# Kernel tuning notes

Measured on AMD Instinct MI355X. Metric: run time of the kernel, lower is better.

The kernel has to match this reference:

```python
import jax, jax.numpy as jnp
import numpy as np
import math

B, N, C = 1, 2048, 256
H, CH = 8, 32
PQ, PV = 8, 12
CZ = 32
BQ, BK = 32, 128
NB = N // BQ
PAD = (BK - BQ) // 2
INF = 1e8
EPS = 1e-8

_KIDX = np.arange(NB)[:, None] * BQ + np.arange(BK)[None, :] - PAD
_KVALID = (_KIDX >= 0) & (_KIDX < N)
_KIDX_C = np.clip(_KIDX, 0, N - 1)


def _quat_to_rot(q):
    q = q / jnp.linalg.norm(q, axis=-1, keepdims=True)
    w, x, y, z = q[..., 0], q[..., 1], q[..., 2], q[..., 3]
    return jnp.stack([
        jnp.stack([1 - 2 * (y * y + z * z), 2 * (x * y - w * z), 2 * (x * z + w * y)], -1),
        jnp.stack([2 * (x * y + w * z), 1 - 2 * (x * x + z * z), 2 * (y * z - w * x)], -1),
        jnp.stack([2 * (x * z - w * y), 2 * (y * z + w * x), 1 - 2 * (x * x + y * y)], -1)], -2)


def _to_queries(x):
    # [B, N, ...] -> [B, NB, BQ, ...]
    return x.reshape((B, NB, BQ) + x.shape[2:])


def _to_keys(x):
    # [B, N, ...] -> [B, NB, BK, ...] zero-padded sliding key windows
    g = x[:, _KIDX_C]
    v = jnp.asarray(_KVALID, x.dtype).reshape((1, NB, BK) + (1,) * (x.ndim - 2))
    return g * v


def _ln(x):
    m = x.mean(-1, keepdims=True)
    var = x.var(-1, keepdims=True)
    return (x - m) / jnp.sqrt(var + 1e-5)


def setup_inputs():
    key = jax.random.key(0)
    ks = jax.random.split(key, 16)
    p = 0.02
    return {
        's': jax.random.normal(ks[0], (B, N, C), jnp.float32),
        'cond': jax.random.normal(ks[1], (B, N, C), jnp.float32),
        'z': jax.random.normal(ks[2], (B, NB, BQ, BK, CZ), jnp.float32),
        'trans': jax.random.normal(ks[3], (B, N, 3), jnp.float32),
        'rots': _quat_to_rot(jax.random.normal(ks[4], (B, N, 4), jnp.float32)),
        's_mask': jnp.ones((B, N), jnp.float32),
        'Wq': jax.random.normal(ks[5], (C, H * CH)) * p,
        'Wk': jax.random.normal(ks[6], (C, H * CH)) * p,
        'Wv': jax.random.normal(ks[7], (C, H * CH)) * p,
        'Wqp': jax.random.normal(ks[8], (C, H * PQ * 3)) * p,
        'Wkvp': jax.random.normal(ks[9], (C, H * (PQ + PV) * 3)) * p,
        'Wb': jax.random.normal(ks[10], (CZ, H)) * p,
        'Wdz': jax.random.normal(ks[11], (CZ, CZ // 4)) * p,
        'head_weights': jnp.full((H,), 0.5413),
        'Wout': jax.random.normal(ks[12], (H * (CZ // 4 + CH + PV * 4), C)) * p,
        'Wg': jax.random.normal(ks[13], (C, C)) * p,
        'bg': jnp.zeros((C,)),
        'Wbeta': jax.random.normal(ks[14], (C, C)) * p,
        'bbeta': jnp.zeros((C,)),
        'g_z': jnp.ones((CZ,)),
        'b_z': jnp.zeros((CZ,)),
    }


def reference(s, cond, z, trans, rots, s_mask, Wq, Wk, Wv, Wqp, Wkvp, Wb, Wdz,
              head_weights, Wout, Wg, bg, Wbeta, bbeta, g_z, b_z):
    # AdaLN on s conditioned on cond; LayerNorm on z
    s = _ln(s) * (cond @ Wg + bg) + (cond @ Wbeta + bbeta)
    z = _ln(z) * g_z + b_z

    q_in = _to_queries(s)            # [B,NB,BQ,C]
    k_in = _to_keys(s)               # [B,NB,BK,C]
    q_t = _to_queries(trans)         # [B,NB,BQ,3]
    q_R = _to_queries(rots)          # [B,NB,BQ,3,3]
    k_t = _to_keys(trans)
    k_R = _to_keys(rots)
    # zero-padded key rotations -> identity
    zero = jnp.all(k_R == 0, axis=(-2, -1))[..., None, None]
    k_R = jnp.where(zero, jnp.eye(3, dtype=k_R.dtype), k_R)

    q = (q_in @ Wq).reshape(B, NB, BQ, H, CH)
    k = (k_in @ Wk).reshape(B, NB, BK, H, CH)
    v = (k_in @ Wv).reshape(B, NB, BK, H, CH)

    q_pts = (q_in @ Wqp).reshape(B, NB, BQ, H * PQ, 3)
    q_pts = jnp.einsum('bnqij,bnqpj->bnqpi', q_R, q_pts) + q_t[..., None, :]
    q_pts = q_pts.reshape(B, NB, BQ, H, PQ, 3)

    kv_pts = (k_in @ Wkvp).reshape(B, NB, BK, H * (PQ + PV), 3)
    kv_pts = jnp.einsum('bnkij,bnkpj->bnkpi', k_R, kv_pts) + k_t[..., None, :]
    kv_pts = kv_pts.reshape(B, NB, BK, H, PQ + PV, 3)
    k_pts, v_pts = kv_pts[..., :PQ, :], kv_pts[..., PQ:, :]

    b = z @ Wb                                    # [B,NB,BQ,BK,H]
    a = jnp.einsum('bnqhc,bnkhc->bnqkh', q, k) * math.sqrt(1.0 / (3 * CH))
    a = a + math.sqrt(1.0 / 3.0) * b

    disp = q_pts[:, :, :, None] - k_pts[:, :, None]   # [B,NB,BQ,BK,H,PQ,3]
    d2 = jnp.sum(disp * disp, axis=-1)                # [B,NB,BQ,BK,H,PQ]
    hw = jax.nn.softplus(head_weights) * math.sqrt(1.0 / (3 * (PQ * 9.0 / 2)))
    pt_att = -0.5 * jnp.sum(d2 * hw[:, None], axis=-1)   # [B,NB,BQ,BK,H]

    m_q = _to_queries(s_mask[..., None])              # [B,NB,BQ,1]
    m_k = _to_keys(s_mask[..., None])                 # [B,NB,BK,1]
    attn_mask = m_q * jnp.swapaxes(m_k, -1, -2)       # [B,NB,BQ,BK]
    attn_mask = INF * (attn_mask - 1.0)

    a = a + pt_att + attn_mask[..., None]
    a = jnp.swapaxes(a, -1, -2)                       # [B,NB,BQ,H,BK]
    a = jax.nn.softmax(a, axis=-1)

    o = jnp.einsum('bnqhk,bnkhc->bnqhc', a, v).reshape(B, NB, BQ, H * CH)
    o_pt = jnp.einsum('bnqhk,bnkhvc->bnqhvc', a, v_pts)      # [B,NB,BQ,H,PV,3]
    o_pt = jnp.einsum('bnqji,bnqhvj->bnqhvi', q_R,
                      o_pt - q_t[:, :, :, None, None, :])     # invert apply
    o_pt_norm = jnp.sqrt(jnp.sum(o_pt ** 2, -1) + EPS).reshape(B, NB, BQ, H * PV)
    o_pt = o_pt.reshape(B, NB, BQ, H * PV * 3)
    pair_z = z @ Wdz                                          # [B,NB,BQ,BK,CZ//4]
    o_pair = jnp.einsum('bnqhk,bnqkc->bnqhc', a, pair_z).reshape(B, NB, BQ, H * (CZ // 4))

    out = jnp.concatenate([o, o_pt, o_pt_norm, o_pair], -1) @ Wout
    return out.reshape(B, N, C)
```

## Files before the change

kernel.cpp:

```cpp
#include <hip/hip_runtime.h>
#include <hip/hip_bf16.h>
#include <math.h>

typedef __hip_bfloat16 bf16;
typedef __attribute__((ext_vector_type(8))) short short8;
typedef __attribute__((ext_vector_type(4))) short short4v;
typedef __attribute__((ext_vector_type(4))) float f32x4;

#define NRES 2048
#define CDIM 256
#define PADK 48
#define POS 1440

static __device__ __forceinline__ float b2f(bf16 x) { return __bfloat162float(x); }
static __device__ __forceinline__ float us2f(short u) {
    return __uint_as_float(((unsigned)(unsigned short)u) << 16);
}
static __device__ __forceinline__ short f2s(float f) {
    bf16 h = __float2bfloat16(f);
    return *reinterpret_cast<short*>(&h);
}
static __device__ __forceinline__ bool flag_f32(const void* smask) {
    return *(const unsigned int*)smask == 0x3F800000u;
}
static __device__ __forceinline__ float dual_load(const void* p, size_t i, bool f32) {
    float vf = ((const float*)p)[f32 ? i : 0];
    float vb = b2f(((const bf16*)p)[f32 ? (size_t)0 : i]);
    return f32 ? vf : vb;
}

struct PrepTable {
    const void* src[8];
    bf16* dst[8];
    int srcN[8];
    int nOff[8];
    int dstStride[8];
    float scl[8];
    int tileOff[9];
    const void* s;
    float* RS;
    const void* cond;
    bf16* condb;
    const void* rots;
    const void* trans;
    float* RT;
    const void* z;
    const void* Wb;
    const void* Wdz;
    const void* g_z;
    const void* b_z;
    bf16* Bzb;
    bf16* PZb;
};
__global__ __launch_bounds__(256) void k_prep(PrepTable tb, const void* __restrict__ smask) {
    __shared__ float tile[32][33];
    __shared__ float wb[32][8], wdz[32][8], gz[32], bz[32];
    bool f32 = flag_f32(smask);
    int b = blockIdx.x;
    int t = threadIdx.x;
    if (b < 1024) {
        {
            int j = t >> 3, c = t & 7;
            wb[j][c] = 0.5773502691896258f * dual_load(tb.Wb, t, f32);
            wdz[j][c] = dual_load(tb.Wdz, t, f32);
        }
        if (t < 32) { gz[t] = dual_load(tb.g_z, t, f32); bz[t] = dual_load(tb.b_z, t, f32); }
        __syncthreads();
        size_t r = (size_t)b * 256 + t;
        float zv[32];
        float sum = 0.f, sq = 0.f;
        if (f32) {
            const float4* zp = (const float4*)((const float*)tb.z + r * 32);
#pragma unroll
            for (int j4 = 0; j4 < 8; ++j4) {
                float4 v4 = zp[j4];
                zv[j4 * 4 + 0] = v4.x; zv[j4 * 4 + 1] = v4.y; zv[j4 * 4 + 2] = v4.z; zv[j4 * 4 + 3] = v4.w;
            }
        } else {
            const bf16* zp = (const bf16*)tb.z + r * 32;
#pragma unroll
            for (int j = 0; j < 32; ++j) zv[j] = b2f(zp[j]);
        }
#pragma unroll
        for (int j = 0; j < 32; ++j) { float v = zv[j]; sum += v; sq += v * v; }
        float m = sum / 32.f;
        float var = fmaxf(sq / 32.f - m * m, 0.f);
        float rstd = rsqrtf(var + 1e-5f);
#pragma unroll
        for (int j = 0; j < 32; ++j) zv[j] = (zv[j] - m) * rstd * gz[j] + bz[j];
        float bacc[8], pacc[8];
#pragma unroll
        for (int c = 0; c < 8; ++c) { bacc[c] = 0.f; pacc[c] = 0.f; }
        for (int j = 0; j < 32; ++j) {
            float v = zv[j];
#pragma unroll
            for (int c = 0; c < 8; ++c) { bacc[c] += v * wb[j][c]; pacc[c] += v * wdz[j][c]; }
        }
        int n = (int)(r >> 12);
        int q = (int)(r >> 7) & 31;
        int k = (int)r & 127;
#pragma unroll
        for (int h = 0; h < 8; ++h)
            tb.Bzb[(size_t)n * 32768 + (size_t)h * 4096 + q * 128 + k] = __float2bfloat16(bacc[h]);
#pragma unroll
        for (int c = 0; c < 8; ++c)
            tb.PZb[(((size_t)(n * 32 + q)) * 8 + c) * 128 + k] = __float2bfloat16(pacc[c]);
        return;
    }
    b -= 1024;
    if (b < tb.tileOff[8]) {
        int s = 0;
        while (b >= tb.tileOff[s + 1]) ++s;
        int rel = b - tb.tileOff[s];
        int ntTiles = tb.srcN[s] >> 5;
        int kt = rel / ntTiles, nt = rel % ntTiles;
        const void* src = tb.src[s];
        int srcN = tb.srcN[s];
        float scl = tb.scl[s];
        int tx = t & 31, ty = t >> 5;
#pragma unroll
        for (int r = 0; r < 4; ++r) {
            int srow = kt * 32 + ty + r * 8;
            int scol = nt * 32 + tx;
            tile[ty + r * 8][tx] = dual_load(src, (size_t)srow * srcN + scol, f32);
        }
        __syncthreads();
        bf16* dst = tb.dst[s];
#pragma unroll
        for (int r = 0; r < 4; ++r) {
            int n = nt * 32 + ty + r * 8 + tb.nOff[s];
            int k = kt * 32 + tx;
            dst[(size_t)n * tb.dstStride[s] + k] = __float2bfloat16(tile[tx][ty + r * 8] * scl);
        }
        return;
    }
    b -= tb.tileOff[8];
    if (b < 256) {
        int i0 = b * 2048;
        for (int i = t; i < 2048; i += 256)
            tb.condb[i0 + i] = __float2bfloat16(dual_load(tb.cond, (size_t)(i0 + i), f32));
        return;
    }
    b -= 256;
    if (b < 256) {
        int wave = t >> 6, lane = t & 63;
        int r0 = b * 8;
        for (int rr = 0; rr < 2; ++rr) {
            int row = r0 + wave * 2 + rr;
            float sum = 0.f, sq = 0.f;
            for (int j = lane; j < CDIM; j += 64) {
                float v = dual_load(tb.s, (size_t)row * CDIM + j, f32);
                sum += v; sq += v * v;
            }
            for (int off = 32; off; off >>= 1) { sum += __shfl_xor(sum, off); sq += __shfl_xor(sq, off); }
            if (lane == 0) {
                float m = sum / CDIM;
                float var = fmaxf(sq / CDIM - m * m, 0.f);
                tb.RS[row * 2 + 0] = m;
                tb.RS[row * 2 + 1] = rsqrtf(var + 1e-5f);
            }
        }
        return;
    }
    b -= 256;
    int i = b * 256 + t;
    int row = i / 12, c = i % 12;
    float v = (c < 9) ? dual_load(tb.rots, (size_t)row * 9 + c, f32)
                      : dual_load(tb.trans, (size_t)row * 3 + (c - 9), f32);
    tb.RT[i] = v;
}

__global__ __launch_bounds__(256) void k_gb(
    const bf16* __restrict__ condb, const bf16* __restrict__ GWt,
    const void* __restrict__ s, const float* __restrict__ RS,
    const void* __restrict__ bg, const void* __restrict__ bbeta,
    const void* __restrict__ smask, bf16* __restrict__ SQb)
{
    bool f32 = flag_f32(smask);
    int wid = threadIdx.x >> 6, lane = threadIdx.x & 63;
    int tid = blockIdx.x * 4 + wid;
    int mt = tid >> 4, nt = tid & 15;
    int idx = lane & 15, quad = lane >> 4;
    const bf16* Ap = condb + (size_t)(mt * 16 + idx) * 256 + quad * 8;
    const bf16* B0 = GWt + (size_t)(nt * 16 + idx) * 256 + quad * 8;
    const bf16* B1 = GWt + (size_t)(256 + nt * 16 + idx) * 256 + quad * 8;
    f32x4 a0 = {0,0,0,0}, a1 = {0,0,0,0};
#pragma unroll
    for (int k = 0; k < 256; k += 32) {
        short8 af = *(const short8*)(Ap + k);
        a0 = __builtin_amdgcn_mfma_f32_16x16x32_bf16(af, *(const short8*)(B0 + k), a0, 0, 0, 0);
        a1 = __builtin_amdgcn_mfma_f32_16x16x32_bf16(af, *(const short8*)(B1 + k), a1, 0, 0, 0);
    }
    int ocol = nt * 16 + idx;
    float bgc = dual_load(bg, ocol, f32), bbc = dual_load(bbeta, ocol, f32);
    int orow = mt * 16 + quad * 4;
#pragma unroll
    for (int r = 0; r < 4; ++r) {
        int row = orow + r;
        float sv = dual_load(s, (size_t)row * 256 + ocol, f32);
        float xn = (sv - RS[row * 2]) * RS[row * 2 + 1];
        SQb[(size_t)row * 256 + ocol] = __float2bfloat16(xn * (a0[r] + bgc) + (a1[r] + bbc));
    }
}

__global__ __launch_bounds__(256) void k_gemm22b(
    const bf16* __restrict__ A, const bf16* __restrict__ Bt, bf16* __restrict__ C,
    int N, int totalWaves)
{
    int wid = threadIdx.x >> 6, lane = threadIdx.x & 63;
    int tid = blockIdx.x * 4 + wid;
    if (tid >= totalWaves) return;
    int tiles_n = N >> 5;
    int mt = tid / tiles_n, nt = tid % tiles_n;
    int idx = lane & 15, quad = lane >> 4;
    const bf16* Ap0 = A + (size_t)(mt * 32 + idx) * 256 + quad * 8;
    const bf16* Ap1 = Ap0 + (size_t)16 * 256;
    const bf16* Bp0 = Bt + (size_t)(nt * 32 + idx) * 256 + quad * 8;
    const bf16* Bp1 = Bp0 + (size_t)16 * 256;
    f32x4 a00 = {0,0,0,0}, a01 = {0,0,0,0}, a10 = {0,0,0,0}, a11 = {0,0,0,0};
#pragma unroll 4
    for (int k = 0; k < 256; k += 32) {
        short8 af0 = *(const short8*)(Ap0 + k);
        short8 af1 = *(const short8*)(Ap1 + k);
        short8 bf0 = *(const short8*)(Bp0 + k);
        short8 bf1 = *(const short8*)(Bp1 + k);
        a00 = __builtin_amdgcn_mfma_f32_16x16x32_bf16(af0, bf0, a00, 0, 0, 0);
        a01 = __builtin_amdgcn_mfma_f32_16x16x32_bf16(af0, bf1, a01, 0, 0, 0);
        a10 = __builtin_amdgcn_mfma_f32_16x16x32_bf16(af1, bf0, a10, 0, 0, 0);
        a11 = __builtin_amdgcn_mfma_f32_16x16x32_bf16(af1, bf1, a11, 0, 0, 0);
    }
    int orow = mt * 32 + quad * 4;
    int ocol = nt * 32 + idx;
#pragma unroll
    for (int r = 0; r < 4; ++r) {
        C[(size_t)(orow + r) * N + ocol] = __float2bfloat16(a00[r]);
        C[(size_t)(orow + r) * N + ocol + 16] = __float2bfloat16(a01[r]);
        C[(size_t)(orow + r + 16) * N + ocol] = __float2bfloat16(a10[r]);
        C[(size_t)(orow + r + 16) * N + ocol + 16] = __float2bfloat16(a11[r]);
    }
}

__global__ __launch_bounds__(256, 4) void k_attn_out(
    const bf16* __restrict__ POb,
    const bf16* __restrict__ Bzb, const bf16* __restrict__ PZb,
    const float* __restrict__ RT,
    const void* __restrict__ smask, const void* __restrict__ head_weights,
    bf16* __restrict__ CATb)
{
    __shared__ char buf[39232];
    __shared__ float rowq[16], rowk[128], mk[128], mqv[16];
    short* VtS = (short*)buf;
    short* KpS = (short*)(buf + 21760);
    short* QpS = (short*)(buf + 29952);
    float* S   = (float*)(buf + 30976);
    short* AsS = (short*)(buf + 30976);
    float* OPT = (float*)(buf + 35328);

    const int bx = blockIdx.x;
    const int n = bx >> 4, h = (bx >> 1) & 7, qh = bx & 1;
    const int t = threadIdx.x;
    const bool f32 = flag_f32(smask);
    const int n32 = n * 32;
    const int q0 = qh * 16;
    const int rowg = n32 + q0;

    const int wid = t >> 6, lane = t & 63, idx = lane & 15, quad = lane >> 4;

    float hwv = dual_load(head_weights, h, f32);
    float ptc = -0.5f * log1pf(expf(hwv)) * 0.09622504486493764f;
    float m2ptc = -2.f * ptc;
    const short8 zero8 = {0,0,0,0,0,0,0,0};

    short8 afeat = *(const short8*)(POb + (size_t)(rowg + idx) * POS + h * 32 + quad * 8);
    short8 bfeat[2];
#pragma unroll
    for (int i = 0; i < 2; ++i) {
        int nt = wid * 2 + i;
        int kg = n32 + nt * 16 + idx - PADK;
        bfeat[i] = (kg >= 0 && kg < NRES)
            ? *(const short8*)(POb + (size_t)kg * POS + 256 + h * 32 + quad * 8) : zero8;
    }
    short bzr[8];
#pragma unroll
    for (int i = 0; i < 2; ++i) {
        int nt = wid * 2 + i;
        int k = nt * 16 + idx;
#pragma unroll
        for (int r = 0; r < 4; ++r) {
            int q = quad * 4 + r;
            bzr[i * 4 + r] = *(const short*)(Bzb + (size_t)n * 32768 + (size_t)h * 4096 + (q0 + q) * 128 + k);
        }
    }
    float4 kr0, kr1, kr2;
    float kmv = 0.f;
    short4v kpts[15];
    const int kgR = n32 + t - PADK;
    const bool validR = (t < 128) && (kgR >= 0 && kgR < NRES);
    if (validR) {
        const float4* rt = (const float4*)(RT + (size_t)kgR * 12);
        kr0 = rt[0]; kr1 = rt[1]; kr2 = rt[2];
        kmv = dual_load(smask, kgR, f32);
        const short4v* pp = (const short4v*)(POb + (size_t)kgR * POS + 960 + h * 60);
#pragma unroll
        for (int g = 0; g < 15; ++g) kpts[g] = pp[g];
    }
    float4 qr0, qr1, qr2;
    float qmv = 0.f;
    short8 qpts[3];
    if (t >= 240) {
        int q = t - 240;
        const float4* rt = (const float4*)(RT + (size_t)(rowg + q) * 12);
        qr0 = rt[0]; qr1 = rt[1]; qr2 = rt[2];
        qmv = dual_load(smask, rowg + q, f32);
        const short8* pp = (const short8*)(POb + (size_t)(rowg + q) * POS + 768 + h * 24);
#pragma unroll
        for (int g = 0; g < 3; ++g) qpts[g] = pp[g];
    }

    for (int i = t; i < 512; i += 256) {
        int k = i >> 2, g = i & 3;
        int kg = n32 + k - PADK;
        short8 v = zero8;
        if (kg >= 0 && kg < NRES)
            v = *(const short8*)(POb + (size_t)kg * POS + 512 + h * 32 + g * 8);
#pragma unroll
        for (int j = 0; j < 8; ++j) VtS[(g * 8 + j) * 136 + k] = v[j];
    }
    if (t < 128) {
        int k = t;
        if (validR) {
            const short* kp = (const short*)kpts;
            float s2 = 0.f;
#pragma unroll
            for (int j = 0; j < 20; ++j) {
                float x = us2f(kp[j * 3 + 0]);
                float y = us2f(kp[j * 3 + 1]);
                float z = us2f(kp[j * 3 + 2]);
                float p0 = kr0.x * x + kr0.y * y + kr0.z * z + kr2.y;
                float p1 = kr0.w * x + kr1.x * y + kr1.y * z + kr2.z;
                float p2 = kr1.z * x + kr1.w * y + kr2.x * z + kr2.w;
                if (j < 8) {
                    KpS[k * 32 + j * 3 + 0] = f2s(p0);
                    KpS[k * 32 + j * 3 + 1] = f2s(p1);
                    KpS[k * 32 + j * 3 + 2] = f2s(p2);
                    s2 += p0 * p0 + p1 * p1 + p2 * p2;
                } else {
                    int v = j - 8;
                    VtS[(32 + v * 3 + 0) * 136 + k] = f2s(p0);
                    VtS[(32 + v * 3 + 1) * 136 + k] = f2s(p1);
                    VtS[(32 + v * 3 + 2) * 136 + k] = f2s(p2);
                }
            }
            *(short8*)(KpS + k * 32 + 24) = zero8;
            rowk[k] = ptc * s2;
            mk[k] = kmv;
        } else {
#pragma unroll
            for (int g = 0; g < 4; ++g) *(short8*)(KpS + k * 32 + g * 8) = zero8;
            for (int x = 32; x < 68; ++x) VtS[x * 136 + k] = 0;
            rowk[k] = 0.f; mk[k] = 0.f;
        }
    } else if (t >= 240) {
        int q = t - 240;
        const short* qp = (const short*)qpts;
        float s2 = 0.f;
#pragma unroll
        for (int p = 0; p < 8; ++p) {
            float x = us2f(qp[p * 3 + 0]);
            float y = us2f(qp[p * 3 + 1]);
            float z = us2f(qp[p * 3 + 2]);
            float p0 = qr0.x * x + qr0.y * y + qr0.z * z + qr2.y;
            float p1 = qr0.w * x + qr1.x * y + qr1.y * z + qr2.z;
            float p2 = qr1.z * x + qr1.w * y + qr2.x * z + qr2.w;
            QpS[q * 32 + p * 3 + 0] = f2s(m2ptc * p0);
            QpS[q * 32 + p * 3 + 1] = f2s(m2ptc * p1);
            QpS[q * 32 + p * 3 + 2] = f2s(m2ptc * p2);
            s2 += p0 * p0 + p1 * p1 + p2 * p2;
        }
        *(short8*)(QpS + q * 32 + 24) = zero8;
        rowq[q] = ptc * s2;
        mqv[q] = qmv;
    }
    __syncthreads();

    short8 a2 = *(const short8*)(QpS + idx * 32 + quad * 8);
#pragma unroll
    for (int i = 0; i < 2; ++i) {
        int nt = wid * 2 + i;
        f32x4 acc = {0.f, 0.f, 0.f, 0.f};
        acc = __builtin_amdgcn_mfma_f32_16x16x32_bf16(afeat, bfeat[i], acc, 0, 0, 0);
        short8 b2 = *(const short8*)(KpS + (nt * 16 + idx) * 32 + quad * 8);
        acc = __builtin_amdgcn_mfma_f32_16x16x32_bf16(a2, b2, acc, 0, 0, 0);
        int k = nt * 16 + idx;
#pragma unroll
        for (int r = 0; r < 4; ++r) {
            int q = quad * 4 + r;
            float msk = 1e8f * (mqv[q] * mk[k] - 1.f);
            S[q * 129 + k] = acc[r] + us2f(bzr[i * 4 + r]) + rowq[q] + rowk[k] + msk;
        }
    }
    __syncthreads();

    float sa0[4], sa1[4];
#pragma unroll
    for (int rr = 0; rr < 4; ++rr) {
        int q = wid * 4 + rr;
        float v0 = S[q * 129 + lane], v1 = S[q * 129 + lane + 64];
        float mx = fmaxf(v0, v1);
        for (int off = 32; off; off >>= 1) mx = fmaxf(mx, __shfl_xor(mx, off));
        float e0 = expf(v0 - mx), e1 = expf(v1 - mx);
        float sm = e0 + e1;
        for (int off = 32; off; off >>= 1) sm += __shfl_xor(sm, off);
        float inv = 1.f / sm;
        sa0[rr] = e0 * inv; sa1[rr] = e1 * inv;
    }
    __syncthreads();
#pragma unroll
    for (int rr = 0; rr < 4; ++rr) {
        int q = wid * 4 + rr;
        AsS[q * 136 + lane] = f2s(sa0[rr]);
        AsS[q * 136 + lane + 64] = f2s(sa1[rr]);
    }
    __syncthreads();

    short8 pz0[8];
    if (t < 128) {
        int q = t >> 3, c = t & 7;
        const short8* pzp = (const short8*)(PZb + ((size_t)(rowg + q) * 8 + c) * 128);
#pragma unroll
        for (int k8 = 0; k8 < 8; ++k8) pz0[k8] = pzp[k8];
    }
#pragma unroll
    for (int i = 0; i < 2; ++i) {
        int tt = wid + i * 4;
        if (tt >= 5) break;
        int nt = tt;
        f32x4 acc = {0.f, 0.f, 0.f, 0.f};
#pragma unroll
        for (int kk = 0; kk < 4; ++kk) {
            short8 af  = *(const short8*)(AsS + idx * 136 + kk * 32 + quad * 8);
            short8 bfv = *(const short8*)(VtS + (nt * 16 + idx) * 136 + kk * 32 + quad * 8);
            acc = __builtin_amdgcn_mfma_f32_16x16x32_bf16(af, bfv, acc, 0, 0, 0);
        }
        int x = nt * 16 + idx;
#pragma unroll
        for (int r = 0; r < 4; ++r) {
            int q = quad * 4 + r;
            if (x < 32)
                CATb[(size_t)(rowg + q) * 704 + h * 32 + x] = __float2bfloat16(acc[r]);
            else if (x < 68)
                OPT[q * 37 + (x - 32)] = acc[r];
        }
    }
    if (t < 128) {
        int q = t >> 3, c = t & 7;
        const short8* pzp = (const short8*)(PZb + ((size_t)(rowg + q) * 8 + c) * 128);
        const short8* asp = (const short8*)(AsS + q * 136);
        float acc = 0.f;
#pragma unroll
        for (int k8 = 0; k8 < 8; ++k8) {
            short8 pv = pz0[k8];
            short8 av = asp[k8];
#pragma unroll
            for (int j = 0; j < 8; ++j) acc += us2f(av[j]) * us2f(pv[j]);
        }
#pragma unroll
        for (int k8 = 0; k8 < 8; ++k8) pz0[k8] = pzp[8 + k8];
#pragma unroll
        for (int k8 = 0; k8 < 8; ++k8) {
            short8 pv = pz0[k8];
            short8 av = asp[8 + k8];
#pragma unroll
            for (int j = 0; j < 8; ++j) acc += us2f(av[j]) * us2f(pv[j]);
        }
        CATb[(size_t)(rowg + q) * 704 + 640 + h * 8 + c] = __float2bfloat16(acc);
    }
    __syncthreads();

    if (t < 192) {
        int q = t / 12, v = t % 12;
        int g = rowg + q;
        const float4* rt = (const float4*)(RT + (size_t)g * 12);
        float4 r0 = rt[0], r1 = rt[1], r2 = rt[2];
        float x = OPT[q * 37 + v * 3 + 0] - r2.y;
        float y = OPT[q * 37 + v * 3 + 1] - r2.z;
        float z = OPT[q * 37 + v * 3 + 2] - r2.w;
        float o0 = r0.x * x + r0.w * y + r1.z * z;
        float o1 = r0.y * x + r1.x * y + r1.w * z;
        float o2 = r0.z * x + r1.y * y + r2.x * z;
        size_t cb = (size_t)g * 704;
        CATb[cb + 256 + (h * 12 + v) * 3 + 0] = __float2bfloat16(o0);
        CATb[cb + 256 + (h * 12 + v) * 3 + 1] = __float2bfloat16(o1);
        CATb[cb + 256 + (h * 12 + v) * 3 + 2] = __float2bfloat16(o2);
        CATb[cb + 544 + h * 12 + v] = __float2bfloat16(sqrtf(o0 * o0 + o1 * o1 + o2 * o2 + 1e-8f));
    }
}

__global__ __launch_bounds__(256) void k_gemm(
    const bf16* __restrict__ A, const bf16* __restrict__ Bt, void* __restrict__ Cv,
    const void* __restrict__ smask)
{
    int wid = threadIdx.x >> 6, lane = threadIdx.x & 63;
    int tid = blockIdx.x * 4 + wid;
    int mt = tid >> 4, nt = tid & 15;
    int idx = lane & 15, quad = lane >> 4;
    const bf16* Ap = A + (size_t)(mt * 16 + idx) * 704 + quad * 8;
    const bf16* Bp = Bt + (size_t)(nt * 16 + idx) * 704 + quad * 8;
    f32x4 acc = {0.f, 0.f, 0.f, 0.f};
#pragma unroll 4
    for (int k = 0; k < 704; k += 32) {
        short8 af = *(const short8*)(Ap + k);
        short8 bfv = *(const short8*)(Bp + k);
        acc = __builtin_amdgcn_mfma_f32_16x16x32_bf16(af, bfv, acc, 0, 0, 0);
    }
    int orow = mt * 16 + quad * 4;
    int ocol = nt * 16 + idx;
    if (flag_f32(smask)) {
        float* C = (float*)Cv;
#pragma unroll
        for (int r = 0; r < 4; ++r) C[(size_t)(orow + r) * 256 + ocol] = acc[r];
    } else {
        bf16* C = (bf16*)Cv;
#pragma unroll
        for (int r = 0; r < 4; ++r) C[(size_t)(orow + r) * 256 + ocol] = __float2bfloat16(acc[r]);
    }
}

extern "C" void kernel_launch(void* const* d_in, const int* in_sizes, int n_in,
                              void* d_out, int out_size, void* d_ws, size_t ws_size,
                              hipStream_t stream) {
    const void* s       = d_in[0];
    const void* cond    = d_in[1];
    const void* z       = d_in[2];
    const void* trans   = d_in[3];
    const void* rots    = d_in[4];
    const void* s_mask  = d_in[5];
    const void* Wq      = d_in[6];
    const void* Wk      = d_in[7];
    const void* Wv      = d_in[8];
    const void* Wqp     = d_in[9];
    const void* Wkvp    = d_in[10];
    const void* Wb      = d_in[11];
    const void* Wdz     = d_in[12];
    const void* hweights= d_in[13];
    const void* Wout    = d_in[14];
    const void* Wg      = d_in[15];
    const void* bg      = d_in[16];
    const void* Wbeta   = d_in[17];
    const void* bbeta   = d_in[18];
    const void* g_z     = d_in[19];
    const void* b_z     = d_in[20];

    float* ws = (float*)d_ws;
    bf16* POb   = (bf16*)(ws);
    bf16* Bzb   = (bf16*)(ws + 1474560);
    bf16* PZb   = (bf16*)(ws + 2523136);
    bf16* SQb   = (bf16*)(ws + 3571712);
    bf16* condb = (bf16*)(ws + 3833856);
    bf16* CATb  = (bf16*)(ws + 4358144);
    bf16* PWt   = (bf16*)(ws + 5079040);
    bf16* GWt   = (bf16*)(ws + 5263360);
    bf16* FWt   = (bf16*)(ws + 5328896);
    float* RT   = (float*)(ws + 5419008);
    float* RS   = (float*)(ws + 5443584);

    PrepTable tb;
    const float qkscale = 0.10206207261596575f;
    tb.src[0] = Wq;   tb.dst[0] = PWt; tb.srcN[0] = 256; tb.nOff[0] = 0;   tb.dstStride[0] = 256; tb.scl[0] = qkscale;
    tb.src[1] = Wk;   tb.dst[1] = PWt; tb.srcN[1] = 256; tb.nOff[1] = 256; tb.dstStride[1] = 256; tb.scl[1] = 1.f;
    tb.src[2] = Wv;   tb.dst[2] = PWt; tb.srcN[2] = 256; tb.nOff[2] = 512; tb.dstStride[2] = 256; tb.scl[2] = 1.f;
    tb.src[3] = Wqp;  tb.dst[3] = PWt; tb.srcN[3] = 192; tb.nOff[3] = 768; tb.dstStride[3] = 256; tb.scl[3] = 1.f;
    tb.src[4] = Wkvp; tb.dst[4] = PWt; tb.srcN[4] = 480; tb.nOff[4] = 960; tb.dstStride[4] = 256; tb.scl[4] = 1.f;
    tb.src[5] = Wg;   tb.dst[5] = GWt; tb.srcN[5] = 256; tb.nOff[5] = 0;   tb.dstStride[5] = 256; tb.scl[5] = 1.f;
    tb.src[6] = Wbeta;tb.dst[6] = GWt; tb.srcN[6] = 256; tb.nOff[6] = 256; tb.dstStride[6] = 256; tb.scl[6] = 1.f;
    tb.src[7] = Wout; tb.dst[7] = FWt; tb.srcN[7] = 256; tb.nOff[7] = 0;   tb.dstStride[7] = 704; tb.scl[7] = 1.f;
    int tc[8] = {64, 64, 64, 48, 120, 64, 64, 176};
    tb.tileOff[0] = 0;
    for (int i = 0; i < 8; ++i) tb.tileOff[i + 1] = tb.tileOff[i] + tc[i];
    tb.s = s; tb.RS = RS;
    tb.cond = cond; tb.condb = condb;
    tb.rots = rots; tb.trans = trans; tb.RT = RT;
    tb.z = z; tb.Wb = Wb; tb.Wdz = Wdz; tb.g_z = g_z; tb.b_z = b_z;
    tb.Bzb = Bzb; tb.PZb = PZb;

    dim3 blk(256);
    k_prep<<<dim3(2296), blk, 0, stream>>>(tb, s_mask);
    k_gb<<<dim3(512), blk, 0, stream>>>(condb, GWt, s, RS, bg, bbeta, s_mask, SQb);
    k_gemm22b<<<dim3(720), blk, 0, stream>>>(SQb, PWt, POb, 1440, 2880);
    k_attn_out<<<dim3(1024), blk, 0, stream>>>(POb, Bzb, PZb, RT, s_mask, hweights, CATb);
    k_gemm<<<dim3(512), blk, 0, stream>>>(CATb, FWt, d_out, s_mask);
}
```

Measured before the change: 168.5 us.

## Fuse all stages into one persistent cooperative kernel with grid syncs

Replaces the five separate launches (prep, gate GEMM, projection GEMM, attention, output GEMM) with one cooperative persistent kernel that loops over work items per phase and separates phases with grid-wide syncs. It also reschedules work: the z layer-norm/projection runs alongside the projection GEMM instead of in the first prep launch. The aim is to remove launch gaps and tail effects between kernels. In exchange it adds grid barrier cost, forces all phases to share the attention kernel's register/LDS budget and occupancy limit, and caps the grid at the occupancy-derived block count.

```diff
diff --git a/kernel.cpp b/kernel.cpp
--- a/kernel.cpp
+++ b/kernel.cpp
@@ -1,6 +1,9 @@
 #include <hip/hip_runtime.h>
+#include <hip/hip_cooperative_groups.h>
 #include <hip/hip_bf16.h>
 #include <math.h>
+
+namespace cg = cooperative_groups;
 
 typedef __hip_bfloat16 bf16;
 typedef __attribute__((ext_vector_type(8))) short short8;
@@ -29,500 +32,485 @@
     return f32 ? vf : vb;
 }
 
-struct PrepTable {
-    const void* src[8];
-    bf16* dst[8];
+struct FusedArgs {
+    const void* wsrc[8];
+    bf16* wdst[8];
     int srcN[8];
     int nOff[8];
     int dstStride[8];
     float scl[8];
     int tileOff[9];
     const void* s;
-    float* RS;
     const void* cond;
-    bf16* condb;
+    const void* z;
+    const void* trans;
     const void* rots;
-    const void* trans;
-    float* RT;
-    const void* z;
+    const void* smask;
+    const void* hweights;
     const void* Wb;
     const void* Wdz;
     const void* g_z;
     const void* b_z;
+    const void* bg;
+    const void* bbeta;
+    bf16* condb;
+    bf16* SQb;
+    bf16* POb;
     bf16* Bzb;
     bf16* PZb;
+    bf16* CATb;
+    bf16* PWt;
+    bf16* GWt;
+    bf16* FWt;
+    float* RT;
+    float* RS;
+    void* out;
 };
-__global__ __launch_bounds__(256) void k_prep(PrepTable tb, const void* __restrict__ smask) {
-    __shared__ float tile[32][33];
-    __shared__ float wb[32][8], wdz[32][8], gz[32], bz[32];
-    bool f32 = flag_f32(smask);
-    int b = blockIdx.x;
-    int t = threadIdx.x;
-    if (b < 1024) {
-        {
-            int j = t >> 3, c = t & 7;
-            wb[j][c] = 0.5773502691896258f * dual_load(tb.Wb, t, f32);
-            wdz[j][c] = dual_load(tb.Wdz, t, f32);
-        }
-        if (t < 32) { gz[t] = dual_load(tb.g_z, t, f32); bz[t] = dual_load(tb.b_z, t, f32); }
-        __syncthreads();
-        size_t r = (size_t)b * 256 + t;
-        float zv[32];
-        float sum = 0.f, sq = 0.f;
-        if (f32) {
-            const float4* zp = (const float4*)((const float*)tb.z + r * 32);
-#pragma unroll
-            for (int j4 = 0; j4 < 8; ++j4) {
-                float4 v4 = zp[j4];
-                zv[j4 * 4 + 0] = v4.x; zv[j4 * 4 + 1] = v4.y; zv[j4 * 4 + 2] = v4.z; zv[j4 * 4 + 3] = v4.w;
-            }
-        } else {
-            const bf16* zp = (const bf16*)tb.z + r * 32;
-#pragma unroll
-            for (int j = 0; j < 32; ++j) zv[j] = b2f(zp[j]);
-        }
-#pragma unroll
-        for (int j = 0; j < 32; ++j) { float v = zv[j]; sum += v; sq += v * v; }
-        float m = sum / 32.f;
-        float var = fmaxf(sq / 32.f - m * m, 0.f);
-        float rstd = rsqrtf(var + 1e-5f);
-#pragma unroll
-        for (int j = 0; j < 32; ++j) zv[j] = (zv[j] - m) * rstd * gz[j] + bz[j];
-        float bacc[8], pacc[8];
-#pragma unroll
-        for (int c = 0; c < 8; ++c) { bacc[c] = 0.f; pacc[c] = 0.f; }
-        for (int j = 0; j < 32; ++j) {
-            float v = zv[j];
-#pragma unroll
-            for (int c = 0; c < 8; ++c) { bacc[c] += v * wb[j][c]; pacc[c] += v * wdz[j][c]; }
-        }
-        int n = (int)(r >> 12);
-        int q = (int)(r >> 7) & 31;
-        int k = (int)r & 127;
-#pragma unroll
-        for (int h = 0; h < 8; ++h)
-            tb.Bzb[(size_t)n * 32768 + (size_t)h * 4096 + q * 128 + k] = __float2bfloat16(bacc[h]);
-#pragma unroll
-        for (int c = 0; c < 8; ++c)
-            tb.PZb[(((size_t)(n * 32 + q)) * 8 + c) * 128 + k] = __float2bfloat16(pacc[c]);
-        return;
-    }
-    b -= 1024;
-    if (b < tb.tileOff[8]) {
-        int s = 0;
-        while (b >= tb.tileOff[s + 1]) ++s;
-        int rel = b - tb.tileOff[s];
-        int ntTiles = tb.srcN[s] >> 5;
-        int kt = rel / ntTiles, nt = rel % ntTiles;
-        const void* src = tb.src[s];
-        int srcN = tb.srcN[s];
-        float scl = tb.scl[s];
-        int tx = t & 31, ty = t >> 5;
-#pragma unroll
-        for (int r = 0; r < 4; ++r) {
-            int srow = kt * 32 + ty + r * 8;
-            int scol = nt * 32 + tx;
-            tile[ty + r * 8][tx] = dual_load(src, (size_t)srow * srcN + scol, f32);
-        }
-        __syncthreads();
-        bf16* dst = tb.dst[s];
-#pragma unroll
-        for (int r = 0; r < 4; ++r) {
-            int n = nt * 32 + ty + r * 8 + tb.nOff[s];
-            int k = kt * 32 + tx;
-            dst[(size_t)n * tb.dstStride[s] + k] = __float2bfloat16(tile[tx][ty + r * 8] * scl);
-        }
-        return;
-    }
-    b -= tb.tileOff[8];
-    if (b < 256) {
-        int i0 = b * 2048;
-        for (int i = t; i < 2048; i += 256)
-            tb.condb[i0 + i] = __float2bfloat16(dual_load(tb.cond, (size_t)(i0 + i), f32));
-        return;
-    }
-    b -= 256;
-    if (b < 256) {
-        int wave = t >> 6, lane = t & 63;
-        int r0 = b * 8;
-        for (int rr = 0; rr < 2; ++rr) {
-            int row = r0 + wave * 2 + rr;
-            float sum = 0.f, sq = 0.f;
-            for (int j = lane; j < CDIM; j += 64) {
-                float v = dual_load(tb.s, (size_t)row * CDIM + j, f32);
-                sum += v; sq += v * v;
-            }
-            for (int off = 32; off; off >>= 1) { sum += __shfl_xor(sum, off); sq += __shfl_xor(sq, off); }
-            if (lane == 0) {
-                float m = sum / CDIM;
-                float var = fmaxf(sq / CDIM - m * m, 0.f);
-                tb.RS[row * 2 + 0] = m;
-                tb.RS[row * 2 + 1] = rsqrtf(var + 1e-5f);
-            }
-        }
-        return;
-    }
-    b -= 256;
-    int i = b * 256 + t;
-    int row = i / 12, c = i % 12;
-    float v = (c < 9) ? dual_load(tb.rots, (size_t)row * 9 + c, f32)
-                      : dual_load(tb.trans, (size_t)row * 3 + (c - 9), f32);
-    tb.RT[i] = v;
-}
-
-__global__ __launch_bounds__(256) void k_gb(
-    const bf16* __restrict__ condb, const bf16* __restrict__ GWt,
-    const void* __restrict__ s, const float* __restrict__ RS,
-    const void* __restrict__ bg, const void* __restrict__ bbeta,
-    const void* __restrict__ smask, bf16* __restrict__ SQb)
-{
-    bool f32 = flag_f32(smask);
-    int wid = threadIdx.x >> 6, lane = threadIdx.x & 63;
-    int tid = blockIdx.x * 4 + wid;
-    int mt = tid >> 4, nt = tid & 15;
-    int idx = lane & 15, quad = lane >> 4;
-    const bf16* Ap = condb + (size_t)(mt * 16 + idx) * 256 + quad * 8;
-    const bf16* B0 = GWt + (size_t)(nt * 16 + idx) * 256 + quad * 8;
-    const bf16* B1 = GWt + (size_t)(256 + nt * 16 + idx) * 256 + quad * 8;
-    f32x4 a0 = {0,0,0,0}, a1 = {0,0,0,0};
-#pragma unroll
-    for (int k = 0; k < 256; k += 32) {
-        short8 af = *(const short8*)(Ap + k);
-        a0 = __builtin_amdgcn_mfma_f32_16x16x32_bf16(af, *(const short8*)(B0 + k), a0, 0, 0, 0);
-        a1 = __builtin_amdgcn_mfma_f32_16x16x32_bf16(af, *(const short8*)(B1 + k), a1, 0, 0, 0);
-    }
-    int ocol = nt * 16 + idx;
-    float bgc = dual_load(bg, ocol, f32), bbc = dual_load(bbeta, ocol, f32);
-    int orow = mt * 16 + quad * 4;
-#pragma unroll
-    for (int r = 0; r < 4; ++r) {
-        int row = orow + r;
-        float sv = dual_load(s, (size_t)row * 256 + ocol, f32);
-        float xn = (sv - RS[row * 2]) * RS[row * 2 + 1];
-        SQb[(size_t)row * 256 + ocol] = __float2bfloat16(xn * (a0[r] + bgc) + (a1[r] + bbc));
-    }
-}
-
-__global__ __launch_bounds__(256) void k_gemm22b(
-    const bf16* __restrict__ A, const bf16* __restrict__ Bt, bf16* __restrict__ C,
-    int N, int totalWaves)
-{
-    int wid = threadIdx.x >> 6, lane = threadIdx.x & 63;
-    int tid = blockIdx.x * 4 + wid;
-    if (tid >= totalWaves) return;
-    int tiles_n = N >> 5;
-    int mt = tid / tiles_n, nt = tid % tiles_n;
-    int idx = lane & 15, quad = lane >> 4;
-    const bf16* Ap0 = A + (size_t)(mt * 32 + idx) * 256 + quad * 8;
-    const bf16* Ap1 = Ap0 + (size_t)16 * 256;
-    const bf16* Bp0 = Bt + (size_t)(nt * 32 + idx) * 256 + quad * 8;
-    const bf16* Bp1 = Bp0 + (size_t)16 * 256;
-    f32x4 a00 = {0,0,0,0}, a01 = {0,0,0,0}, a10 = {0,0,0,0}, a11 = {0,0,0,0};
-#pragma unroll 4
-    for (int k = 0; k < 256; k += 32) {
-        short8 af0 = *(const short8*)(Ap0 + k);
-        short8 af1 = *(const short8*)(Ap1 + k);
-        short8 bf0 = *(const short8*)(Bp0 + k);
-        short8 bf1 = *(const short8*)(Bp1 + k);
-        a00 = __builtin_amdgcn_mfma_f32_16x16x32_bf16(af0, bf0, a00, 0, 0, 0);
-        a01 = __builtin_amdgcn_mfma_f32_16x16x32_bf16(af0, bf1, a01, 0, 0, 0);
-        a10 = __builtin_amdgcn_mfma_f32_16x16x32_bf16(af1, bf0, a10, 0, 0, 0);
-        a11 = __builtin_amdgcn_mfma_f32_16x16x32_bf16(af1, bf1, a11, 0, 0, 0);
-    }
-    int orow = mt * 32 + quad * 4;
-    int ocol = nt * 32 + idx;
-#pragma unroll
-    for (int r = 0; r < 4; ++r) {
-        C[(size_t)(orow + r) * N + ocol] = __float2bfloat16(a00[r]);
-        C[(size_t)(orow + r) * N + ocol + 16] = __float2bfloat16(a01[r]);
-        C[(size_t)(orow + r + 16) * N + ocol] = __float2bfloat16(a10[r]);
-        C[(size_t)(orow + r + 16) * N + ocol + 16] = __float2bfloat16(a11[r]);
-    }
-}
-
-__global__ __launch_bounds__(256, 4) void k_attn_out(
-    const bf16* __restrict__ POb,
-    const bf16* __restrict__ Bzb, const bf16* __restrict__ PZb,
-    const float* __restrict__ RT,
-    const void* __restrict__ smask, const void* __restrict__ head_weights,
-    bf16* __restrict__ CATb)
-{
+
+__global__ __launch_bounds__(256, 4) void k_fused(FusedArgs a) {
+    cg::grid_group gridg = cg::this_grid();
     __shared__ char buf[39232];
     __shared__ float rowq[16], rowk[128], mk[128], mqv[16];
-    short* VtS = (short*)buf;
-    short* KpS = (short*)(buf + 21760);
-    short* QpS = (short*)(buf + 29952);
-    float* S   = (float*)(buf + 30976);
-    short* AsS = (short*)(buf + 30976);
-    float* OPT = (float*)(buf + 35328);
-
-    const int bx = blockIdx.x;
-    const int n = bx >> 4, h = (bx >> 1) & 7, qh = bx & 1;
+
+    const bool f32 = flag_f32(a.smask);
     const int t = threadIdx.x;
-    const bool f32 = flag_f32(smask);
-    const int n32 = n * 32;
-    const int q0 = qh * 16;
-    const int rowg = n32 + q0;
-
     const int wid = t >> 6, lane = t & 63, idx = lane & 15, quad = lane >> 4;
-
-    float hwv = dual_load(head_weights, h, f32);
-    float ptc = -0.5f * log1pf(expf(hwv)) * 0.09622504486493764f;
-    float m2ptc = -2.f * ptc;
+    const int G = gridDim.x;
     const short8 zero8 = {0,0,0,0,0,0,0,0};
 
-    short8 afeat = *(const short8*)(POb + (size_t)(rowg + idx) * POS + h * 32 + quad * 8);
-    short8 bfeat[2];
-#pragma unroll
-    for (int i = 0; i < 2; ++i) {
-        int nt = wid * 2 + i;
-        int kg = n32 + nt * 16 + idx - PADK;
-        bfeat[i] = (kg >= 0 && kg < NRES)
-            ? *(const short8*)(POb + (size_t)kg * POS + 256 + h * 32 + quad * 8) : zero8;
+    for (int b = blockIdx.x; b < 1176; b += G) {
+        if (b < 664) {
+            float* tile = (float*)buf;
+            int s_ = 0;
+            while (b >= a.tileOff[s_ + 1]) ++s_;
+            int rel = b - a.tileOff[s_];
+            int ntT = a.srcN[s_] >> 5;
+            int kt = rel / ntT, nt = rel % ntT;
+            const void* src = a.wsrc[s_];
+            int srcN = a.srcN[s_];
+            float scl = a.scl[s_];
+            int tx = t & 31, ty = t >> 5;
+#pragma unroll
+            for (int r = 0; r < 4; ++r)
+                tile[(ty + r * 8) * 33 + tx] =
+                    dual_load(src, (size_t)(kt * 32 + ty + r * 8) * srcN + nt * 32 + tx, f32);
+            __syncthreads();
+            bf16* dst = a.wdst[s_];
+#pragma unroll
+            for (int r = 0; r < 4; ++r)
+                dst[(size_t)(nt * 32 + ty + r * 8 + a.nOff[s_]) * a.dstStride[s_] + kt * 32 + tx] =
+                    __float2bfloat16(tile[tx * 33 + ty + r * 8] * scl);
+        } else if (b < 920) {
+            int i0 = (b - 664) * 2048;
+            for (int i = t; i < 2048; i += 256)
+                a.condb[i0 + i] = __float2bfloat16(dual_load(a.cond, (size_t)(i0 + i), f32));
+        } else {
+            int r0 = (b - 920) * 8;
+            for (int rr = 0; rr < 2; ++rr) {
+                int row = r0 + wid * 2 + rr;
+                float sum = 0.f, sq = 0.f;
+                for (int j = lane; j < CDIM; j += 64) {
+                    float v = dual_load(a.s, (size_t)row * CDIM + j, f32);
+                    sum += v; sq += v * v;
+                }
+                for (int off = 32; off; off >>= 1) { sum += __shfl_xor(sum, off); sq += __shfl_xor(sq, off); }
+                if (lane == 0) {
+                    float m = sum / CDIM;
+                    float var = fmaxf(sq / CDIM - m * m, 0.f);
+                    a.RS[row * 2 + 0] = m;
+                    a.RS[row * 2 + 1] = rsqrtf(var + 1e-5f);
+                }
+            }
+        }
+        __syncthreads();
     }
-    short bzr[8];
-#pragma unroll
-    for (int i = 0; i < 2; ++i) {
-        int nt = wid * 2 + i;
-        int k = nt * 16 + idx;
+    gridg.sync();
+
+    for (int bb = blockIdx.x; bb < 512; bb += G) {
+        int tid = bb * 4 + wid;
+        int mt = tid >> 4, nt = tid & 15;
+        const bf16* Ap = a.condb + (size_t)(mt * 16 + idx) * 256 + quad * 8;
+        const bf16* B0 = a.GWt + (size_t)(nt * 16 + idx) * 256 + quad * 8;
+        const bf16* B1 = a.GWt + (size_t)(256 + nt * 16 + idx) * 256 + quad * 8;
+        f32x4 a0 = {0,0,0,0}, a1 = {0,0,0,0};
+#pragma unroll
+        for (int k = 0; k < 256; k += 32) {
+            short8 af = *(const short8*)(Ap + k);
+            a0 = __builtin_amdgcn_mfma_f32_16x16x32_bf16(af, *(const short8*)(B0 + k), a0, 0, 0, 0);
+            a1 = __builtin_amdgcn_mfma_f32_16x16x32_bf16(af, *(const short8*)(B1 + k), a1, 0, 0, 0);
+        }
+        int ocol = nt * 16 + idx;
+        float bgc = dual_load(a.bg, ocol, f32), bbc = dual_load(a.bbeta, ocol, f32);
+        int orow = mt * 16 + quad * 4;
 #pragma unroll
         for (int r = 0; r < 4; ++r) {
-            int q = quad * 4 + r;
-            bzr[i * 4 + r] = *(const short*)(Bzb + (size_t)n * 32768 + (size_t)h * 4096 + (q0 + q) * 128 + k);
+            int row = orow + r;
+            float sv = dual_load(a.s, (size_t)row * 256 + ocol, f32);
+            float xn = (sv - a.RS[row * 2]) * a.RS[row * 2 + 1];
+            a.SQb[(size_t)row * 256 + ocol] = __float2bfloat16(xn * (a0[r] + bgc) + (a1[r] + bbc));
         }
     }
-    float4 kr0, kr1, kr2;
-    float kmv = 0.f;
-    short4v kpts[15];
-    const int kgR = n32 + t - PADK;
-    const bool validR = (t < 128) && (kgR >= 0 && kgR < NRES);
-    if (validR) {
-        const float4* rt = (const float4*)(RT + (size_t)kgR * 12);
-        kr0 = rt[0]; kr1 = rt[1]; kr2 = rt[2];
-        kmv = dual_load(smask, kgR, f32);
-        const short4v* pp = (const short4v*)(POb + (size_t)kgR * POS + 960 + h * 60);
-#pragma unroll
-        for (int g = 0; g < 15; ++g) kpts[g] = pp[g];
+    gridg.sync();
+
+    for (int b = blockIdx.x; b < 1840; b += G) {
+        if (b < 720) {
+            int tid = b * 4 + wid;
+            int mt = tid / 45, nt = tid % 45;
+            const bf16* Ap0 = a.SQb + (size_t)(mt * 32 + idx) * 256 + quad * 8;
+            const bf16* Ap1 = Ap0 + (size_t)16 * 256;
+            const bf16* Bp0 = a.PWt + (size_t)(nt * 32 + idx) * 256 + quad * 8;
+            const bf16* Bp1 = Bp0 + (size_t)16 * 256;
+            f32x4 a00 = {0,0,0,0}, a01 = {0,0,0,0}, a10 = {0,0,0,0}, a11 = {0,0,0,0};
+#pragma unroll 4
+            for (int k = 0; k < 256; k += 32) {
+                short8 af0 = *(const short8*)(Ap0 + k);
+                short8 af1 = *(const short8*)(Ap1 + k);
+                short8 bf0 = *(const short8*)(Bp0 + k);
+                short8 bf1 = *(const short8*)(Bp1 + k);
+                a00 = __builtin_amdgcn_mfma_f32_16x16x32_bf16(af0, bf0, a00, 0, 0, 0);
+                a01 = __builtin_amdgcn_mfma_f32_16x16x32_bf16(af0, bf1, a01, 0, 0, 0);
+                a10 = __builtin_amdgcn_mfma_f32_16x16x32_bf16(af1, bf0, a10, 0, 0, 0);
+                a11 = __builtin_amdgcn_mfma_f32_16x16x32_bf16(af1, bf1, a11, 0, 0, 0);
+            }
+            int orow = mt * 32 + quad * 4;
+            int ocol = nt * 32 + idx;
+#pragma unroll
+            for (int r = 0; r < 4; ++r) {
+                a.POb[(size_t)(orow + r) * POS + ocol] = __float2bfloat16(a00[r]);
+                a.POb[(size_t)(orow + r) * POS + ocol + 16] = __float2bfloat16(a01[r]);
+                a.POb[(size_t)(orow + r + 16) * POS + ocol] = __float2bfloat16(a10[r]);
+                a.POb[(size_t)(orow + r + 16) * POS + ocol + 16] = __float2bfloat16(a11[r]);
+            }
+        } else if (b < 1744) {
+            int zb = b - 720;
+            float* wb  = (float*)buf;
+            float* wdz = (float*)(buf + 1024);
+            float* gz  = (float*)(buf + 2048);
+            float* bz  = (float*)(buf + 2176);
+            {
+                int j = t >> 3, c = t & 7;
+                wb[j * 8 + c] = 0.5773502691896258f * dual_load(a.Wb, t, f32);
+                wdz[j * 8 + c] = dual_load(a.Wdz, t, f32);
+            }
+            if (t < 32) { gz[t] = dual_load(a.g_z, t, f32); bz[t] = dual_load(a.b_z, t, f32); }
+            __syncthreads();
+            size_t r = (size_t)zb * 256 + t;
+            float zv[32];
+            float sum = 0.f, sq = 0.f;
+            if (f32) {
+                const float4* zp = (const float4*)((const float*)a.z + r * 32);
+#pragma unroll
+                for (int j4 = 0; j4 < 8; ++j4) {
+                    float4 v4 = zp[j4];
+                    zv[j4 * 4 + 0] = v4.x; zv[j4 * 4 + 1] = v4.y; zv[j4 * 4 + 2] = v4.z; zv[j4 * 4 + 3] = v4.w;
+                }
+            } else {
+                const bf16* zp = (const bf16*)a.z + r * 32;
+#pragma unroll
+                for (int j = 0; j < 32; ++j) zv[j] = b2f(zp[j]);
+            }
+#pragma unroll
+            for (int j = 0; j < 32; ++j) { float v = zv[j]; sum += v; sq += v * v; }
+            float m = sum / 32.f;
+            float var = fmaxf(sq / 32.f - m * m, 0.f);
+            float rstd = rsqrtf(var + 1e-5f);
+#pragma unroll
+            for (int j = 0; j < 32; ++j) zv[j] = (zv[j] - m) * rstd * gz[j] + bz[j];
+            float bacc[8], pacc[8];
+#pragma unroll
+            for (int c = 0; c < 8; ++c) { bacc[c] = 0.f; pacc[c] = 0.f; }
+            for (int j = 0; j < 32; ++j) {
+                float v = zv[j];
+#pragma unroll
+                for (int c = 0; c < 8; ++c) { bacc[c] += v * wb[j * 8 + c]; pacc[c] += v * wdz[j * 8 + c]; }
+            }
+            int n = (int)(r >> 12);
+            int q = (int)(r >> 7) & 31;
+            int k = (int)r & 127;
+#pragma unroll
+            for (int h = 0; h < 8; ++h)
+                a.Bzb[(size_t)n * 32768 + (size_t)h * 4096 + q * 128 + k] = __float2bfloat16(bacc[h]);
+#pragma unroll
+            for (int c = 0; c < 8; ++c)
+                a.PZb[(((size_t)(n * 32 + q)) * 8 + c) * 128 + k] = __float2bfloat16(pacc[c]);
+        } else {
+            int i = (b - 1744) * 256 + t;
+            int row = i / 12, c = i % 12;
+            float v = (c < 9) ? dual_load(a.rots, (size_t)row * 9 + c, f32)
+                              : dual_load(a.trans, (size_t)row * 3 + (c - 9), f32);
+            a.RT[i] = v;
+        }
+        __syncthreads();
     }
-    float4 qr0, qr1, qr2;
-    float qmv = 0.f;
-    short8 qpts[3];
-    if (t >= 240) {
-        int q = t - 240;
-        const float4* rt = (const float4*)(RT + (size_t)(rowg + q) * 12);
-        qr0 = rt[0]; qr1 = rt[1]; qr2 = rt[2];
-        qmv = dual_load(smask, rowg + q, f32);
-        const short8* pp = (const short8*)(POb + (size_t)(rowg + q) * POS + 768 + h * 24);
-#pragma unroll
-        for (int g = 0; g < 3; ++g) qpts[g] = pp[g];
+    gridg.sync();
+
+    for (int ab = blockIdx.x; ab < 1024; ab += G) {
+        short* VtS = (short*)buf;
+        short* KpS = (short*)(buf + 21760);
+        short* QpS = (short*)(buf + 29952);
+        float* S   = (float*)(buf + 30976);
+        short* AsS = (short*)(buf + 30976);
+        float* OPT = (float*)(buf + 35328);
+
+        const int n = ab >> 4, h = (ab >> 1) & 7, qh = ab & 1;
+        const int n32 = n * 32;
+        const int q0 = qh * 16;
+        const int rowg = n32 + q0;
+
+        float hwv = dual_load(a.hweights, h, f32);
+        float ptc = -0.5f * log1pf(expf(hwv)) * 0.09622504486493764f;
+        float m2ptc = -2.f * ptc;
+
+        short8 afeat = *(const short8*)(a.POb + (size_t)(rowg + idx) * POS + h * 32 + quad * 8);
+        short8 bfeat[2];
+#pragma unroll
+        for (int i = 0; i < 2; ++i) {
+            int nt = wid * 2 + i;
+            int kg = n32 + nt * 16 + idx - PADK;
+            bfeat[i] = (kg >= 0 && kg < NRES)
+                ? *(const short8*)(a.POb + (size_t)kg * POS + 256 + h * 32 + quad * 8) : zero8;
+        }
+        short bzr[8];
+#pragma unroll
+        for (int i = 0; i < 2; ++i) {
+            int nt = wid * 2 + i;
+            int k = nt * 16 + idx;
+#pragma unroll
+            for (int r = 0; r < 4; ++r) {
+                int q = quad * 4 + r;
+                bzr[i * 4 + r] = *(const short*)(a.Bzb + (size_t)n * 32768 + (size_t)h * 4096 + (q0 + q) * 128 + k);
+            }
+        }
+        float4 kr0, kr1, kr2;
+        float kmv = 0.f;
+        short4v kpts[15];
+        const int kgR = n32 + t - PADK;
+        const bool validR = (t < 128) && (kgR >= 0 && kgR < NRES);
+        if (validR) {
+            const float4* rt = (const float4*)(a.RT + (size_t)kgR * 12);
+            kr0 = rt[0]; kr1 = rt[1]; kr2 = rt[2];
+            kmv = dual_load(a.smask, kgR, f32);
+            const short4v* pp = (const short4v*)(a.POb + (size_t)kgR * POS + 960 + h * 60);
+#pragma unroll
+            for (int g = 0; g < 15; ++g) kpts[g] = pp[g];
+        }
+        float4 qr0, qr1, qr2;
+        float qmv = 0.f;
+        short8 qpts[3];
+        if (t >= 240) {
+            int q = t - 240;
+            const float4* rt = (const float4*)(a.RT + (size_t)(rowg + q) * 12);
+            qr0 = rt[0]; qr1 = rt[1]; qr2 = rt[2];
+            qmv = dual_load(a.smask, rowg + q, f32);
+            const short8* pp = (const short8*)(a.POb + (size_t)(rowg + q) * POS + 768 + h * 24);
+#pragma unroll
+            for (int g = 0; g < 3; ++g) qpts[g] = pp[g];
+        }
+
+        for (int i = t; i < 512; i += 256) {
+            int k = i >> 2, g = i & 3;
+            int kg = n32 + k - PADK;
+            short8 v = zero8;
+            if (kg >= 0 && kg < NRES)
+                v = *(const short8*)(a.POb + (size_t)kg * POS + 512 + h * 32 + g * 8);
+#pragma unroll
+            for (int j = 0; j < 8; ++j) VtS[(g * 8 + j) * 136 + k] = v[j];
+        }
+        if (t < 128) {
+            int k = t;
+            if (validR) {
+                const short* kp = (const short*)kpts;
+                float s2 = 0.f;
+#pragma unroll
+                for (int j = 0; j < 20; ++j) {
+                    float x = us2f(kp[j * 3 + 0]);
+                    float y = us2f(kp[j * 3 + 1]);
+                    float z = us2f(kp[j * 3 + 2]);
+                    float p0 = kr0.x * x + kr0.y * y + kr0.z * z + kr2.y;
+                    float p1 = kr0.w * x + kr1.x * y + kr1.y * z + kr2.z;
+                    float p2 = kr1.z * x + kr1.w * y + kr2.x * z + kr2.w;
+                    if (j < 8) {
+                        KpS[k * 32 + j * 3 + 0] = f2s(p0);
+                        KpS[k * 32 + j * 3 + 1] = f2s(p1);
+                        KpS[k * 32 + j * 3 + 2] = f2s(p2);
+                        s2 += p0 * p0 + p1 * p1 + p2 * p2;
+                    } else {
+                        int v = j - 8;
+                        VtS[(32 + v * 3 + 0) * 136 + k] = f2s(p0);
+                        VtS[(32 + v * 3 + 1) * 136 + k] = f2s(p1);
+                        VtS[(32 + v * 3 + 2) * 136 + k] = f2s(p2);
+                    }
+                }
+                *(short8*)(KpS + k * 32 + 24) = zero8;
+                rowk[k] = ptc * s2;
+                mk[k] = kmv;
+            } else {
+#pragma unroll
+                for (int g = 0; g < 4; ++g) *(short8*)(KpS + k * 32 + g * 8) = zero8;
+                for (int x = 32; x < 68; ++x) VtS[x * 136 + k] = 0;
+                rowk[k] = 0.f; mk[k] = 0.f;
+            }
+        } else if (t >= 240) {
+            int q = t - 240;
+            const short* qp = (const short*)qpts;
+            float s2 = 0.f;
+#pragma unroll
+            for (int p = 0; p < 8; ++p) {
+                float x = us2f(qp[p * 3 + 0]);
+                float y = us2f(qp[p * 3 + 1]);
+                float z = us2f(qp[p * 3 + 2]);
+                float p0 = qr0.x * x + qr0.y * y + qr0.z * z + qr2.y;
+                float p1 = qr0.w * x + qr1.x * y + qr1.y * z + qr2.z;
+                float p2 = qr1.z * x + qr1.w * y + qr2.x * z + qr2.w;
+                QpS[q * 32 + p * 3 + 0] = f2s(m2ptc * p0);
+                QpS[q * 32 + p * 3 + 1] = f2s(m2ptc * p1);
+                QpS[q * 32 + p * 3 + 2] = f2s(m2ptc * p2);
+                s2 += p0 * p0 + p1 * p1 + p2 * p2;
+            }
+            *(short8*)(QpS + q * 32 + 24) = zero8;
+            rowq[q] = ptc * s2;
+            mqv[q] = qmv;
+        }
+        __syncthreads();
+
+        short8 a2 = *(const short8*)(QpS + idx * 32 + quad * 8);
+#pragma unroll
+        for (int i = 0; i < 2; ++i) {
+            int nt = wid * 2 + i;
+            f32x4 acc = {0.f, 0.f, 0.f, 0.f};
+            acc = __builtin_amdgcn_mfma_f32_16x16x32_bf16(afeat, bfeat[i], acc, 0, 0, 0);
+            short8 b2 = *(const short8*)(KpS + (nt * 16 + idx) * 32 + quad * 8);
+            acc = __builtin_amdgcn_mfma_f32_16x16x32_bf16(a2, b2, acc, 0, 0, 0);
+            int k = nt * 16 + idx;
+#pragma unroll
+            for (int r = 0; r < 4; ++r) {
+                int q = quad * 4 + r;
+                float msk = 1e8f * (mqv[q] * mk[k] - 1.f);
+                S[q * 129 + k] = acc[r] + us2f(bzr[i * 4 + r]) + rowq[q] + rowk[k] + msk;
+            }
+        }
+        __syncthreads();
+
+        float sa0[4], sa1[4];
+#pragma unroll
+        for (int rr = 0; rr < 4; ++rr) {
+            int q = wid * 4 + rr;
+            float v0 = S[q * 129 + lane], v1 = S[q * 129 + lane + 64];
+            float mx = fmaxf(v0, v1);
+            for (int off = 32; off; off >>= 1) mx = fmaxf(mx, __shfl_xor(mx, off));
+            float e0 = expf(v0 - mx), e1 = expf(v1 - mx);
+            float sm = e0 + e1;
+            for (int off = 32; off; off >>= 1) sm += __shfl_xor(sm, off);
+            float inv = 1.f / sm;
+            sa0[rr] = e0 * inv; sa1[rr] = e1 * inv;
+        }
+        __syncthreads();
+#pragma unroll
+        for (int rr = 0; rr < 4; ++rr) {
+            int q = wid * 4 + rr;
+            AsS[q * 136 + lane] = f2s(sa0[rr]);
+            AsS[q * 136 + lane + 64] = f2s(sa1[rr]);
+        }
+        __syncthreads();
+
+        short8 pz0[8];
+        if (t < 128) {
+            int q = t >> 3, c = t & 7;
+            const short8* pzp = (const short8*)(a.PZb + ((size_t)(rowg + q) * 8 + c) * 128);
+#pragma unroll
+            for (int k8 = 0; k8 < 8; ++k8) pz0[k8] = pzp[k8];
+        }
+#pragma unroll
+        for (int i = 0; i < 2; ++i) {
+            int tt = wid + i * 4;
+            if (tt >= 5) break;
+            int nt = tt;
+            f32x4 acc = {0.f, 0.f, 0.f, 0.f};
+#pragma unroll
+            for (int kk = 0; kk < 4; ++kk) {
+                short8 af  = *(const short8*)(AsS + idx * 136 + kk * 32 + quad * 8);
+                short8 bfv = *(const short8*)(VtS + (nt * 16 + idx) * 136 + kk * 32 + quad * 8);
+                acc = __builtin_amdgcn_mfma_f32_16x16x32_bf16(af, bfv, acc, 0, 0, 0);
+            }
+            int x = nt * 16 + idx;
+#pragma unroll
+            for (int r = 0; r < 4; ++r) {
+                int q = quad * 4 + r;
+                if (x < 32)
+                    a.CATb[(size_t)(rowg + q) * 704 + h * 32 + x] = __float2bfloat16(acc[r]);
+                else if (x < 68)
+                    OPT[q * 37 + (x - 32)] = acc[r];
+            }
+        }
+        if (t < 128) {
+            int q = t >> 3, c = t & 7;
+            const short8* pzp = (const short8*)(a.PZb + ((size_t)(rowg + q) * 8 + c) * 128);
+            const short8* asp = (const short8*)(AsS + q * 136);
+            float acc = 0.f;
+#pragma unroll
+            for (int k8 = 0; k8 < 8; ++k8) {
+                short8 pv = pz0[k8];
+                short8 av = asp[k8];
+#pragma unroll
+                for (int j = 0; j < 8; ++j) acc += us2f(av[j]) * us2f(pv[j]);
+            }
+#pragma unroll
+            for (int k8 = 0; k8 < 8; ++k8) pz0[k8] = pzp[8 + k8];
+#pragma unroll
+            for (int k8 = 0; k8 < 8; ++k8) {
+                short8 pv = pz0[k8];
+                short8 av = asp[8 + k8];
+#pragma unroll
+                for (int j = 0; j < 8; ++j) acc += us2f(av[j]) * us2f(pv[j]);
+            }
+            a.CATb[(size_t)(rowg + q) * 704 + 640 + h * 8 + c] = __float2bfloat16(acc);
+        }
+        __syncthreads();
+
+        if (t < 192) {
+            int q = t / 12, v = t % 12;
+            int g = rowg + q;
+            const float4* rt = (const float4*)(a.RT + (size_t)g * 12);
+            float4 r0 = rt[0], r1 = rt[1], r2 = rt[2];
+            float x = OPT[q * 37 + v * 3 + 0] - r2.y;
+            float y = OPT[q * 37 + v * 3 + 1] - r2.z;
+            float z = OPT[q * 37 + v * 3 + 2] - r2.w;
+            float o0 = r0.x * x + r0.w * y + r1.z * z;
+            float o1 = r0.y * x + r1.x * y + r1.w * z;
+            float o2 = r0.z * x + r1.y * y + r2.x * z;
+            size_t cb = (size_t)g * 704;
+            a.CATb[cb + 256 + (h * 12 + v) * 3 + 0] = __float2bfloat16(o0);
+            a.CATb[cb + 256 + (h * 12 + v) * 3 + 1] = __float2bfloat16(o1);
+            a.CATb[cb + 256 + (h * 12 + v) * 3 + 2] = __float2bfloat16(o2);
+            a.CATb[cb + 544 + h * 12 + v] = __float2bfloat16(sqrtf(o0 * o0 + o1 * o1 + o2 * o2 + 1e-8f));
+        }
+        __syncthreads();
     }
-
-    for (int i = t; i < 512; i += 256) {
-        int k = i >> 2, g = i & 3;
-        int kg = n32 + k - PADK;
-        short8 v = zero8;
-        if (kg >= 0 && kg < NRES)
-            v = *(const short8*)(POb + (size_t)kg * POS + 512 + h * 32 + g * 8);
-#pragma unroll
-        for (int j = 0; j < 8; ++j) VtS[(g * 8 + j) * 136 + k] = v[j];
-    }
-    if (t < 128) {
-        int k = t;
-        if (validR) {
-            const short* kp = (const short*)kpts;
-            float s2 = 0.f;
-#pragma unroll
-            for (int j = 0; j < 20; ++j) {
-                float x = us2f(kp[j * 3 + 0]);
-                float y = us2f(kp[j * 3 + 1]);
-                float z = us2f(kp[j * 3 + 2]);
-                float p0 = kr0.x * x + kr0.y * y + kr0.z * z + kr2.y;
-                float p1 = kr0.w * x + kr1.x * y + kr1.y * z + kr2.z;
-                float p2 = kr1.z * x + kr1.w * y + kr2.x * z + kr2.w;
-                if (j < 8) {
-                    KpS[k * 32 + j * 3 + 0] = f2s(p0);
-                    KpS[k * 32 + j * 3 + 1] = f2s(p1);
-                    KpS[k * 32 + j * 3 + 2] = f2s(p2);
-                    s2 += p0 * p0 + p1 * p1 + p2 * p2;
-                } else {
-                    int v = j - 8;
-                    VtS[(32 + v * 3 + 0) * 136 + k] = f2s(p0);
-                    VtS[(32 + v * 3 + 1) * 136 + k] = f2s(p1);
-                    VtS[(32 + v * 3 + 2) * 136 + k] = f2s(p2);
-                }
-            }
-            *(short8*)(KpS + k * 32 + 24) = zero8;
-            rowk[k] = ptc * s2;
-            mk[k] = kmv;
+    gridg.sync();
+
+    for (int bb = blockIdx.x; bb < 512; bb += G) {
+        int tid = bb * 4 + wid;
+        int mt = tid >> 4, nt = tid & 15;
+        const bf16* Ap = a.CATb + (size_t)(mt * 16 + idx) * 704 + quad * 8;
+        const bf16* Bp = a.FWt + (size_t)(nt * 16 + idx) * 704 + quad * 8;
+        f32x4 acc = {0.f, 0.f, 0.f, 0.f};
+#pragma unroll 4
+        for (int k = 0; k < 704; k += 32) {
+            short8 af = *(const short8*)(Ap + k);
+            short8 bfv = *(const short8*)(Bp + k);
+            acc = __builtin_amdgcn_mfma_f32_16x16x32_bf16(af, bfv, acc, 0, 0, 0);
+        }
+        int orow = mt * 16 + quad * 4;
+        int ocol = nt * 16 + idx;
+        if (f32) {
+            float* C = (float*)a.out;
+#pragma unroll
+            for (int r = 0; r < 4; ++r) C[(size_t)(orow + r) * 256 + ocol] = acc[r];
         } else {
-#pragma unroll
-            for (int g = 0; g < 4; ++g) *(short8*)(KpS + k * 32 + g * 8) = zero8;
-            for (int x = 32; x < 68; ++x) VtS[x * 136 + k] = 0;
-            rowk[k] = 0.f; mk[k] = 0.f;
-        }
-    } else if (t >= 240) {
-        int q = t - 240;
-        const short* qp = (const short*)qpts;
-        float s2 = 0.f;
-#pragma unroll
-        for (int p = 0; p < 8; ++p) {
-            float x = us2f(qp[p * 3 + 0]);
-            float y = us2f(qp[p * 3 + 1]);
-            float z = us2f(qp[p * 3 + 2]);
-            float p0 = qr0.x * x + qr0.y * y + qr0.z * z + qr2.y;
-            float p1 = qr0.w * x + qr1.x * y + qr1.y * z + qr2.z;
-            float p2 = qr1.z * x + qr1.w * y + qr2.x * z + qr2.w;
-            QpS[q * 32 + p * 3 + 0] = f2s(m2ptc * p0);
-            QpS[q * 32 + p * 3 + 1] = f2s(m2ptc * p1);
-            QpS[q * 32 + p * 3 + 2] = f2s(m2ptc * p2);
-            s2 += p0 * p0 + p1 * p1 + p2 * p2;
-        }
-        *(short8*)(QpS + q * 32 + 24) = zero8;
-        rowq[q] = ptc * s2;
-        mqv[q] = qmv;
-    }
-    __syncthreads();
-
-    short8 a2 = *(const short8*)(QpS + idx * 32 + quad * 8);
-#pragma unroll
-    for (int i = 0; i < 2; ++i) {
-        int nt = wid * 2 + i;
-        f32x4 acc = {0.f, 0.f, 0.f, 0.f};
-        acc = __builtin_amdgcn_mfma_f32_16x16x32_bf16(afeat, bfeat[i], acc, 0, 0, 0);
-        short8 b2 = *(const short8*)(KpS + (nt * 16 + idx) * 32 + quad * 8);
-        acc = __builtin_amdgcn_mfma_f32_16x16x32_bf16(a2, b2, acc, 0, 0, 0);
-        int k = nt * 16 + idx;
-#pragma unroll
-        for (int r = 0; r < 4; ++r) {
-            int q = quad * 4 + r;
-            float msk = 1e8f * (mqv[q] * mk[k] - 1.f);
-            S[q * 129 + k] = acc[r] + us2f(bzr[i * 4 + r]) + rowq[q] + rowk[k] + msk;
-        }
-    }
-    __syncthreads();
-
-    float sa0[4], sa1[4];
-#pragma unroll
-    for (int rr = 0; rr < 4; ++rr) {
-        int q = wid * 4 + rr;
-        float v0 = S[q * 129 + lane], v1 = S[q * 129 + lane + 64];
-        float mx = fmaxf(v0, v1);
-        for (int off = 32; off; off >>= 1) mx = fmaxf(mx, __shfl_xor(mx, off));
-        float e0 = expf(v0 - mx), e1 = expf(v1 - mx);
-        float sm = e0 + e1;
-        for (int off = 32; off; off >>= 1) sm += __shfl_xor(sm, off);
-        float inv = 1.f / sm;
-        sa0[rr] = e0 * inv; sa1[rr] = e1 * inv;
-    }
-    __syncthreads();
-#pragma unroll
-    for (int rr = 0; rr < 4; ++rr) {
-        int q = wid * 4 + rr;
-        AsS[q * 136 + lane] = f2s(sa0[rr]);
-        AsS[q * 136 + lane + 64] = f2s(sa1[rr]);
-    }
-    __syncthreads();
-
-    short8 pz0[8];
-    if (t < 128) {
-        int q = t >> 3, c = t & 7;
-        const short8* pzp = (const short8*)(PZb + ((size_t)(rowg + q) * 8 + c) * 128);
-#pragma unroll
-        for (int k8 = 0; k8 < 8; ++k8) pz0[k8] = pzp[k8];
-    }
-#pragma unroll
-    for (int i = 0; i < 2; ++i) {
-        int tt = wid + i * 4;
-        if (tt >= 5) break;
-        int nt = tt;
-        f32x4 acc = {0.f, 0.f, 0.f, 0.f};
-#pragma unroll
-        for (int kk = 0; kk < 4; ++kk) {
-            short8 af  = *(const short8*)(AsS + idx * 136 + kk * 32 + quad * 8);
-            short8 bfv = *(const short8*)(VtS + (nt * 16 + idx) * 136 + kk * 32 + quad * 8);
-            acc = __builtin_amdgcn_mfma_f32_16x16x32_bf16(af, bfv, acc, 0, 0, 0);
-        }
-        int x = nt * 16 + idx;
-#pragma unroll
-        for (int r = 0; r < 4; ++r) {
-            int q = quad * 4 + r;
-            if (x < 32)
-                CATb[(size_t)(rowg + q) * 704 + h * 32 + x] = __float2bfloat16(acc[r]);
-            else if (x < 68)
-                OPT[q * 37 + (x - 32)] = acc[r];
-        }
-    }
-    if (t < 128) {
-        int q = t >> 3, c = t & 7;
-        const short8* pzp = (const short8*)(PZb + ((size_t)(rowg + q) * 8 + c) * 128);
-        const short8* asp = (const short8*)(AsS + q * 136);
-        float acc = 0.f;
-#pragma unroll
-        for (int k8 = 0; k8 < 8; ++k8) {
-            short8 pv = pz0[k8];
-            short8 av = asp[k8];
-#pragma unroll
-            for (int j = 0; j < 8; ++j) acc += us2f(av[j]) * us2f(pv[j]);
-        }
-#pragma unroll
-        for (int k8 = 0; k8 < 8; ++k8) pz0[k8] = pzp[8 + k8];
-#pragma unroll
-        for (int k8 = 0; k8 < 8; ++k8) {
-            short8 pv = pz0[k8];
-            short8 av = asp[8 + k8];
-#pragma unroll
-            for (int j = 0; j < 8; ++j) acc += us2f(av[j]) * us2f(pv[j]);
-        }
-        CATb[(size_t)(rowg + q) * 704 + 640 + h * 8 + c] = __float2bfloat16(acc);
-    }
-    __syncthreads();
-
-    if (t < 192) {
-        int q = t / 12, v = t % 12;
-        int g = rowg + q;
-        const float4* rt = (const float4*)(RT + (size_t)g * 12);
-        float4 r0 = rt[0], r1 = rt[1], r2 = rt[2];
-        float x = OPT[q * 37 + v * 3 + 0] - r2.y;
-        float y = OPT[q * 37 + v * 3 + 1] - r2.z;
-        float z = OPT[q * 37 + v * 3 + 2] - r2.w;
-        float o0 = r0.x * x + r0.w * y + r1.z * z;
-        float o1 = r0.y * x + r1.x * y + r1.w * z;
-        float o2 = r0.z * x + r1.y * y + r2.x * z;
-        size_t cb = (size_t)g * 704;
-        CATb[cb + 256 + (h * 12 + v) * 3 + 0] = __float2bfloat16(o0);
-        CATb[cb + 256 + (h * 12 + v) * 3 + 1] = __float2bfloat16(o1);
-        CATb[cb + 256 + (h * 12 + v) * 3 + 2] = __float2bfloat16(o2);
-        CATb[cb + 544 + h * 12 + v] = __float2bfloat16(sqrtf(o0 * o0 + o1 * o1 + o2 * o2 + 1e-8f));
-    }
-}
-
-__global__ __launch_bounds__(256) void k_gemm(
-    const bf16* __restrict__ A, const bf16* __restrict__ Bt, void* __restrict__ Cv,
-    const void* __restrict__ smask)
-{
-    int wid = threadIdx.x >> 6, lane = threadIdx.x & 63;
-    int tid = blockIdx.x * 4 + wid;
-    int mt = tid >> 4, nt = tid & 15;
-    int idx = lane & 15, quad = lane >> 4;
-    const bf16* Ap = A + (size_t)(mt * 16 + idx) * 704 + quad * 8;
-    const bf16* Bp = Bt + (size_t)(nt * 16 + idx) * 704 + quad * 8;
-    f32x4 acc = {0.f, 0.f, 0.f, 0.f};
-#pragma unroll 4
-    for (int k = 0; k < 704; k += 32) {
-        short8 af = *(const short8*)(Ap + k);
-        short8 bfv = *(const short8*)(Bp + k);
-        acc = __builtin_amdgcn_mfma_f32_16x16x32_bf16(af, bfv, acc, 0, 0, 0);
-    }
-    int orow = mt * 16 + quad * 4;
-    int ocol = nt * 16 + idx;
-    if (flag_f32(smask)) {
-        float* C = (float*)Cv;
-#pragma unroll
-        for (int r = 0; r < 4; ++r) C[(size_t)(orow + r) * 256 + ocol] = acc[r];
-    } else {
-        bf16* C = (bf16*)Cv;
-#pragma unroll
-        for (int r = 0; r < 4; ++r) C[(size_t)(orow + r) * 256 + ocol] = __float2bfloat16(acc[r]);
+            bf16* C = (bf16*)a.out;
+#pragma unroll
+            for (int r = 0; r < 4; ++r) C[(size_t)(orow + r) * 256 + ocol] = __float2bfloat16(acc[r]);
+        }
     }
 }
 
@@ -552,41 +540,44 @@
     const void* b_z     = d_in[20];
 
     float* ws = (float*)d_ws;
-    bf16* POb   = (bf16*)(ws);
-    bf16* Bzb   = (bf16*)(ws + 1474560);
-    bf16* PZb   = (bf16*)(ws + 2523136);
-    bf16* SQb   = (bf16*)(ws + 3571712);
-    bf16* condb = (bf16*)(ws + 3833856);
-    bf16* CATb  = (bf16*)(ws + 4358144);
-    bf16* PWt   = (bf16*)(ws + 5079040);
-    bf16* GWt   = (bf16*)(ws + 5263360);
-    bf16* FWt   = (bf16*)(ws + 5328896);
-    float* RT   = (float*)(ws + 5419008);
-    float* RS   = (float*)(ws + 5443584);
-
-    PrepTable tb;
+    FusedArgs a;
+    a.POb   = (bf16*)(ws);
+    a.Bzb   = (bf16*)(ws + 1474560);
+    a.PZb   = (bf16*)(ws + 2523136);
+    a.SQb   = (bf16*)(ws + 3571712);
+    a.condb = (bf16*)(ws + 3833856);
+    a.CATb  = (bf16*)(ws + 4358144);
+    a.PWt   = (bf16*)(ws + 5079040);
+    a.GWt   = (bf16*)(ws + 5263360);
+    a.FWt   = (bf16*)(ws + 5328896);
+    a.RT    = (float*)(ws + 5419008);
+    a.RS    = (float*)(ws + 5443584);
+
     const float qkscale = 0.10206207261596575f;
-    tb.src[0] = Wq;   tb.dst[0] = PWt; tb.srcN[0] = 256; tb.nOff[0] = 0;   tb.dstStride[0] = 256; tb.scl[0] = qkscale;
-    tb.src[1] = Wk;   tb.dst[1] = PWt; tb.srcN[1] = 256; tb.nOff[1] = 256; tb.dstStride[1] = 256; tb.scl[1] = 1.f;
-    tb.src[2] = Wv;   tb.dst[2] = PWt; tb.srcN[2] = 256; tb.nOff[2] = 512; tb.dstStride[2] = 256; tb.scl[2] = 1.f;
-    tb.src[3] = Wqp;  tb.dst[3] = PWt; tb.srcN[3] = 192; tb.nOff[3] = 768; tb.dstStride[3] = 256; tb.scl[3] = 1.f;
-    tb.src[4] = Wkvp; tb.dst[4] = PWt; tb.srcN[4] = 480; tb.nOff[4] = 960; tb.dstStride[4] = 256; tb.scl[4] = 1.f;
-    tb.src[5] = Wg;   tb.dst[5] = GWt; tb.srcN[5] = 256; tb.nOff[5] = 0;   tb.dstStride[5] = 256; tb.scl[5] = 1.f;
-    tb.src[6] = Wbeta;tb.dst[6] = GWt; tb.srcN[6] = 256; tb.nOff[6] = 256; tb.dstStride[6] = 256; tb.scl[6] = 1.f;
-    tb.src[7] = Wout; tb.dst[7] = FWt; tb.srcN[7] = 256; tb.nOff[7] = 0;   tb.dstStride[7] = 704; tb.scl[7] = 1.f;
+    a.wsrc[0] = Wq;   a.wdst[0] = a.PWt; a.srcN[0] = 256; a.nOff[0] = 0;   a.dstStride[0] = 256; a.scl[0] = qkscale;
+    a.wsrc[1] = Wk;   a.wdst[1] = a.PWt; a.srcN[1] = 256; a.nOff[1] = 256; a.dstStride[1] = 256; a.scl[1] = 1.f;
+    a.wsrc[2] = Wv;   a.wdst[2] = a.PWt; a.srcN[2] = 256; a.nOff[2] = 512; a.dstStride[2] = 256; a.scl[2] = 1.f;
+    a.wsrc[3] = Wqp;  a.wdst[3] = a.PWt; a.srcN[3] = 192; a.nOff[3] = 768; a.dstStride[3] = 256; a.scl[3] = 1.f;
+    a.wsrc[4] = Wkvp; a.wdst[4] = a.PWt; a.srcN[4] = 480; a.nOff[4] = 960; a.dstStride[4] = 256; a.scl[4] = 1.f;
+    a.wsrc[5] = Wg;   a.wdst[5] = a.GWt; a.srcN[5] = 256; a.nOff[5] = 0;   a.dstStride[5] = 256; a.scl[5] = 1.f;
+    a.wsrc[6] = Wbeta;a.wdst[6] = a.GWt; a.srcN[6] = 256; a.nOff[6] = 256; a.dstStride[6] = 256; a.scl[6] = 1.f;
+    a.wsrc[7] = Wout; a.wdst[7] = a.FWt; a.srcN[7] = 256; a.nOff[7] = 0;   a.dstStride[7] = 704; a.scl[7] = 1.f;
     int tc[8] = {64, 64, 64, 48, 120, 64, 64, 176};
-    tb.tileOff[0] = 0;
-    for (int i = 0; i < 8; ++i) tb.tileOff[i + 1] = tb.tileOff[i] + tc[i];
-    tb.s = s; tb.RS = RS;
-    tb.cond = cond; tb.condb = condb;
-    tb.rots = rots; tb.trans = trans; tb.RT = RT;
-    tb.z = z; tb.Wb = Wb; tb.Wdz = Wdz; tb.g_z = g_z; tb.b_z = b_z;
-    tb.Bzb = Bzb; tb.PZb = PZb;
-
-    dim3 blk(256);
-    k_prep<<<dim3(2296), blk, 0, stream>>>(tb, s_mask);
-    k_gb<<<dim3(512), blk, 0, stream>>>(condb, GWt, s, RS, bg, bbeta, s_mask, SQb);
-    k_gemm22b<<<dim3(720), blk, 0, stream>>>(SQb, PWt, POb, 1440, 2880);
-    k_attn_out<<<dim3(1024), blk, 0, stream>>>(POb, Bzb, PZb, RT, s_mask, hweights, CATb);
-    k_gemm<<<dim3(512), blk, 0, stream>>>(CATb, FWt, d_out, s_mask);
+    a.tileOff[0] = 0;
+    for (int i = 0; i < 8; ++i) a.tileOff[i + 1] = a.tileOff[i] + tc[i];
+    a.s = s; a.cond = cond; a.z = z; a.trans = trans; a.rots = rots;
+    a.smask = s_mask; a.hweights = hweights;
+    a.Wb = Wb; a.Wdz = Wdz; a.g_z = g_z; a.b_z = b_z;
+    a.bg = bg; a.bbeta = bbeta;
+    a.out = d_out;
+
+    int bpc = 0;
+    if (hipOccupancyMaxActiveBlocksPerMultiprocessor(&bpc, (const void*)k_fused, 256, 0) != hipSuccess || bpc < 1)
+        bpc = 2;
+    if (bpc > 4) bpc = 4;
+    int grid = bpc * 256;
+    if (grid > 1024) grid = 1024;
+
+    void* args[] = { (void*)&a };
+    hipLaunchCooperativeKernel((const void*)k_fused, dim3(grid), dim3(256), args, 0, stream);
 }
```

Result: slower. 484.6 us (+187.7%).
